# Kernel optimization log

Hardware: AMD Instinct MI355X
Metric: run time of the kernel (lower is better)

## Reference

```python
import jax, jax.numpy as jnp
import numpy as np

BSZ, DIM, SEQ_A, SEQ_B = 16, 768, 1024, 1024


def setup_inputs() -> dict:
    key = jax.random.key(0)
    kA, kB, kU = jax.random.split(key, 3)
    input_A = jax.random.normal(kA, (BSZ, DIM, SEQ_A), dtype=jnp.float32)
    input_B = jax.random.normal(kB, (BSZ, DIM, SEQ_B), dtype=jnp.float32)
    intput_msk = jnp.zeros((BSZ, SEQ_A, SEQ_B), dtype=jnp.float32)  # 0 = on, -inf = off
    U = jax.random.normal(kU, (DIM, DIM), dtype=jnp.float32)
    return {"input_A": input_A, "input_B": input_B, "intput_msk": intput_msk, "U": U}


def reference(input_A, input_B, intput_msk, U):
    # align[b,s,t] = tanh( A[b,:,s]^T U B[b,:,t] )  -> (bsz, seq_A, seq_B)
    align = jnp.einsum("bds,de,bet->bst", input_A, U, input_B)
    align = jnp.tanh(align) + intput_msk
    # per-token scores: max over the other modality's sequence, then softmax
    score_A = jax.nn.softmax(jnp.max(align, axis=2), axis=-1)  # (bsz, seq_A)
    score_B = jax.nn.softmax(jnp.max(align, axis=1), axis=-1)  # (bsz, seq_B)
    output_A = jnp.einsum("bds,bs->bd", input_A, score_A)  # (bsz, dim_A)
    output_B = jnp.einsum("bdt,bt->bd", input_B, score_B)  # (bsz, dim_B)
    return (output_A, output_B)
```

## Files before the change

### kernel.cpp

```cpp
#include <hip/hip_runtime.h>
#include <math.h>

#define BSZ  16
#define DIM  768
#define SEQA 1024
#define SEQB 1024

typedef float f32x4 __attribute__((ext_vector_type(4)));
typedef long long llong;

__device__ inline void gload_lds16(const void* g, void* l) {
    __builtin_amdgcn_global_load_lds(
        (const __attribute__((address_space(1))) void*)g,
        (__attribute__((address_space(3))) void*)l, 16, 0, 0);
}

__device__ inline unsigned enc_key(float f) {
    unsigned u = __float_as_uint(f);
    return (u & 0x80000000u) ? ~u : (u | 0x80000000u);
}
__device__ inline float dec_key(unsigned k) {
    return (k & 0x80000000u) ? __uint_as_float(k ^ 0x80000000u) : __uint_as_float(~k);
}

__device__ inline unsigned pk4_fp8(float a, float b, float c, float d) {
    int v = 0;
    v = __builtin_amdgcn_cvt_pk_fp8_f32(a, b, v, false);
    v = __builtin_amdgcn_cvt_pk_fp8_f32(c, d, v, true);
    return (unsigned)v;
}
__device__ inline unsigned char f2fp8(float a) {
    return (unsigned char)(__builtin_amdgcn_cvt_pk_fp8_f32(a, a, 0, false) & 0xFF);
}
__device__ inline unsigned short f2bf(float f) {
    unsigned u = __float_as_uint(f);
    return (unsigned short)((u + 0x7FFF + ((u >> 16) & 1)) >> 16);
}
__device__ inline float bf2f(unsigned short h) {
    return __uint_as_float((unsigned)h << 16);
}

__device__ inline float fast_tanh(float x) {
    float ax = fabsf(x);
    float u = __expf(-2.0f * ax);
    float th = __fdividef(1.0f - u, 1.0f + u);
    return copysignf(th, x);
}

__global__ __launch_bounds__(256) void t_cast_AB(const float* __restrict__ A,
                                                 const float* __restrict__ B,
                                                 unsigned char* __restrict__ At,
                                                 unsigned char* __restrict__ Bt,
                                                 unsigned short* __restrict__ At16,
                                                 unsigned short* __restrict__ Bt16,
                                                 int w16) {
    __shared__ float tl[64][68];
    const int z = blockIdx.z;
    const float* X = (z < BSZ) ? A : B;
    unsigned char* Y = (z < BSZ) ? At : Bt;
    unsigned short* Y16 = (z < BSZ) ? At16 : Bt16;
    const int b = z & 15;
    const int d0 = blockIdx.y * 64;
    const int s0 = blockIdx.x * 64;
    const int tid = threadIdx.x;
    const int rr = tid >> 4, c4 = tid & 15;
    const float* Xb = X + ((size_t)b * DIM + d0) * SEQA + s0;
#pragma unroll
    for (int i = 0; i < 4; i++) {
        int row = i * 16 + rr;
        float4 v = *(const float4*)&Xb[(size_t)row * SEQA + c4 * 4];
        *(float4*)&tl[row][c4 * 4] = v;
    }
    __syncthreads();
    const int m = tid & 15, sl = tid >> 4;
    unsigned char* Yb = Y + ((size_t)b * SEQA + s0) * DIM + d0;
#pragma unroll
    for (int i = 0; i < 4; i++) {
        int s = sl + 16 * i;
        unsigned v = pk4_fp8(tl[4 * m + 0][s], tl[4 * m + 1][s], tl[4 * m + 2][s], tl[4 * m + 3][s]);
        *(unsigned*)&Yb[(size_t)s * DIM + 4 * m] = v;
    }
    if (w16) {
        unsigned short* Yc = Y16 + ((size_t)b * SEQA + s0) * DIM + d0;
#pragma unroll
        for (int i = 0; i < 4; i++) {
            int s = sl + 16 * i;
            uint2 w;
            w.x = (unsigned)f2bf(tl[4 * m + 0][s]) | ((unsigned)f2bf(tl[4 * m + 1][s]) << 16);
            w.y = (unsigned)f2bf(tl[4 * m + 2][s]) | ((unsigned)f2bf(tl[4 * m + 3][s]) << 16);
            *(uint2*)&Yc[(size_t)s * DIM + 4 * m] = w;
        }
    }
}

__global__ __launch_bounds__(256) void t_cast_U(const float* __restrict__ U,
                                                unsigned char* __restrict__ Ut,
                                                unsigned* __restrict__ keyA,
                                                unsigned* __restrict__ keyB) {
    __shared__ float tl[64][68];
    const int d0 = blockIdx.y * 64;
    const int e0 = blockIdx.x * 64;
    const int tid = threadIdx.x;
    const int bid = blockIdx.y * gridDim.x + blockIdx.x;
    if (bid < 64) {
        int i = bid * 256 + tid;
        keyA[i] = 0u;
        keyB[i] = 0u;
    }
    const int rr = tid >> 4, c4 = tid & 15;
#pragma unroll
    for (int i = 0; i < 4; i++) {
        int row = i * 16 + rr;
        float4 v = *(const float4*)&U[(size_t)(d0 + row) * DIM + e0 + c4 * 4];
        *(float4*)&tl[row][c4 * 4] = v;
    }
    __syncthreads();
    const int m = tid & 15, sl = tid >> 4;
#pragma unroll
    for (int i = 0; i < 4; i++) {
        int e = sl + 16 * i;
        unsigned v = pk4_fp8(tl[4 * m + 0][e], tl[4 * m + 1][e], tl[4 * m + 2][e], tl[4 * m + 3][e]);
        *(unsigned*)&Ut[(size_t)(e0 + e) * DIM + d0 + 4 * m] = v;
    }
}

__device__ inline void stage64(const unsigned char* __restrict__ src, int kbyte0,
                               unsigned char* buf, int wid, int lane) {
    const int grow = lane >> 1;
    const int gcol = ((lane & 1) ^ ((lane >> 3) & 1)) * 16;
#pragma unroll
    for (int h = 0; h < 2; ++h)
        gload_lds16(src + (size_t)(wid * 32 + grow) * DIM + kbyte0 + 32 * h + gcol,
                    buf + h * 4096 + wid * 1024 + lane * 16);
}
__device__ inline llong frag64(const unsigned char* buf, int rowbase, int l15,
                               int quad, int h) {
    int koff = (((quad >> 1) ^ ((l15 >> 2) & 1)) << 4) + (quad & 1) * 8;
    return *(const llong*)(buf + h * 4096 + (rowbase + l15) * 32 + koff);
}

#define NK (DIM / 64)

__global__ __launch_bounds__(256) void k1_ua(const unsigned char* __restrict__ At,
                                             const unsigned char* __restrict__ Ut,
                                             unsigned char* __restrict__ Ct) {
    __shared__ __align__(16) unsigned char As[2][8192];
    __shared__ __align__(16) unsigned char Us[2][8192];
    const int b  = blockIdx.z;
    const int s0 = blockIdx.x * 128;
    const int e0 = blockIdx.y * 128;
    const int tid = threadIdx.x;
    const int lane = tid & 63;
    const int wid = tid >> 6;
    const int wr = wid >> 1, wc = wid & 1;
    const int quad = lane >> 4, l15 = lane & 15;

    const unsigned char* Ab = At + (size_t)(b * SEQA + s0) * DIM;
    const unsigned char* Ub = Ut + (size_t)e0 * DIM;
    f32x4 acc[4][4] = {};

#define K_COMPUTE(BUF)                                                               \
    {                                                                                \
        _Pragma("unroll") for (int h = 0; h < 2; ++h) {                              \
            llong av[4], bv[4];                                                      \
            _Pragma("unroll") for (int i = 0; i < 4; ++i)                            \
                av[i] = frag64(As[BUF], wr * 64 + 16 * i, l15, quad, h);             \
            _Pragma("unroll") for (int j = 0; j < 4; ++j)                            \
                bv[j] = frag64(Us[BUF], wc * 64 + 16 * j, l15, quad, h);             \
            _Pragma("unroll") for (int i = 0; i < 4; ++i)                            \
                _Pragma("unroll") for (int j = 0; j < 4; ++j)                        \
                    acc[i][j] = __builtin_amdgcn_mfma_f32_16x16x32_fp8_fp8(          \
                        av[i], bv[j], acc[i][j], 0, 0, 0);                           \
        }                                                                            \
    }

    stage64(Ab, 0, As[0], wid, lane);
    stage64(Ub, 0, Us[0], wid, lane);
    __syncthreads();
    for (int it = 0; it < NK; it += 2) {
        stage64(Ab, (it + 1) * 64, As[1], wid, lane);
        stage64(Ub, (it + 1) * 64, Us[1], wid, lane);
        K_COMPUTE(0);
        __syncthreads();
        if (it + 2 < NK) {
            stage64(Ab, (it + 2) * 64, As[0], wid, lane);
            stage64(Ub, (it + 2) * 64, Us[0], wid, lane);
        }
        K_COMPUTE(1);
        __syncthreads();
    }
    unsigned char* Cb = Ct + (size_t)b * SEQA * DIM;
#pragma unroll
    for (int i = 0; i < 4; ++i)
#pragma unroll
        for (int j = 0; j < 4; ++j) {
            int e_g = e0 + wc * 64 + 16 * j + l15;
#pragma unroll
            for (int r = 0; r < 4; ++r) {
                int s_g = s0 + wr * 64 + 16 * i + quad * 4 + r;
                Cb[(size_t)s_g * DIM + e_g] = f2fp8(acc[i][j][r]);
            }
        }
}

__global__ __launch_bounds__(256) void k2_align(const unsigned char* __restrict__ Ct,
                                                const unsigned char* __restrict__ Bt,
                                                const float* __restrict__ msk,
                                                unsigned* __restrict__ keyA,
                                                unsigned* __restrict__ keyB) {
    __shared__ __align__(16) unsigned char As[2][8192];
    __shared__ __align__(16) unsigned char Us[2][8192];
    const int b  = blockIdx.z;
    const int t0 = blockIdx.x * 128;
    const int s0 = blockIdx.y * 128;
    const int tid = threadIdx.x;
    const int lane = tid & 63;
    const int wid = tid >> 6;
    const int wr = wid >> 1, wc = wid & 1;
    const int quad = lane >> 4, l15 = lane & 15;

    const unsigned char* Bb = Bt + (size_t)(b * SEQB + t0) * DIM;
    const unsigned char* Cb = Ct + (size_t)(b * SEQA + s0) * DIM;
    f32x4 acc[4][4] = {};

    stage64(Bb, 0, As[0], wid, lane);
    stage64(Cb, 0, Us[0], wid, lane);
    __syncthreads();
    for (int it = 0; it < NK; it += 2) {
        stage64(Bb, (it + 1) * 64, As[1], wid, lane);
        stage64(Cb, (it + 1) * 64, Us[1], wid, lane);
        K_COMPUTE(0);
        __syncthreads();
        if (it + 2 < NK) {
            stage64(Bb, (it + 2) * 64, As[0], wid, lane);
            stage64(Cb, (it + 2) * 64, Us[0], wid, lane);
        }
        K_COMPUTE(1);
        __syncthreads();
    }

    const float* Mb = msk + (size_t)b * SEQA * SEQB;
#pragma unroll
    for (int i = 0; i < 4; ++i)
#pragma unroll
        for (int j = 0; j < 4; ++j) {
            int s_g = s0 + wc * 64 + 16 * j + l15;
            int t_g = t0 + wr * 64 + 16 * i + quad * 4;
            float4 mv = *(const float4*)&Mb[(size_t)s_g * SEQB + t_g];
            acc[i][j][0] = fast_tanh(acc[i][j][0]) + mv.x;
            acc[i][j][1] = fast_tanh(acc[i][j][1]) + mv.y;
            acc[i][j][2] = fast_tanh(acc[i][j][2]) + mv.z;
            acc[i][j][3] = fast_tanh(acc[i][j][3]) + mv.w;
        }
#pragma unroll
    for (int j = 0; j < 4; ++j) {
        float m = -INFINITY;
#pragma unroll
        for (int i = 0; i < 4; ++i)
#pragma unroll
            for (int r = 0; r < 4; ++r) m = fmaxf(m, acc[i][j][r]);
        m = fmaxf(m, __shfl_xor(m, 16));
        m = fmaxf(m, __shfl_xor(m, 32));
        if (quad == 0)
            atomicMax(&keyA[b * SEQA + s0 + wc * 64 + 16 * j + l15], enc_key(m));
    }
#pragma unroll
    for (int i = 0; i < 4; ++i)
#pragma unroll
        for (int r = 0; r < 4; ++r) {
            float m = fmaxf(fmaxf(acc[i][0][r], acc[i][1][r]), fmaxf(acc[i][2][r], acc[i][3][r]));
            m = fmaxf(m, __shfl_xor(m, 1));
            m = fmaxf(m, __shfl_xor(m, 2));
            m = fmaxf(m, __shfl_xor(m, 4));
            m = fmaxf(m, __shfl_xor(m, 8));
            if (l15 == 0)
                atomicMax(&keyB[b * SEQB + t0 + wr * 64 + 16 * i + quad * 4 + r], enc_key(m));
        }
}

__global__ __launch_bounds__(256) void k3_softmax(const unsigned* __restrict__ keyA,
                                                  const unsigned* __restrict__ keyB,
                                                  float* __restrict__ scoreA,
                                                  float* __restrict__ scoreB) {
    const int b = blockIdx.x;
    const bool isA = (blockIdx.y == 0);
    const unsigned* keys = isA ? (keyA + b * SEQA) : (keyB + b * SEQB);
    float* score = isA ? (scoreA + b * SEQA) : (scoreB + b * SEQB);
    __shared__ float sh[4];
    const int tid = threadIdx.x;
    float m[4];
    float mx = -INFINITY;
#pragma unroll
    for (int k = 0; k < 4; k++) {
        m[k] = dec_key(keys[tid + 256 * k]);
        mx = fmaxf(mx, m[k]);
    }
#pragma unroll
    for (int o = 32; o > 0; o >>= 1) mx = fmaxf(mx, __shfl_down(mx, o, 64));
    if ((tid & 63) == 0) sh[tid >> 6] = mx;
    __syncthreads();
    mx = fmaxf(fmaxf(sh[0], sh[1]), fmaxf(sh[2], sh[3]));
    __syncthreads();
    float e[4];
    float sum = 0.f;
#pragma unroll
    for (int k = 0; k < 4; k++) { e[k] = expf(m[k] - mx); sum += e[k]; }
#pragma unroll
    for (int o = 32; o > 0; o >>= 1) sum += __shfl_down(sum, o, 64);
    if ((tid & 63) == 0) sh[tid >> 6] = sum;
    __syncthreads();
    sum = sh[0] + sh[1] + sh[2] + sh[3];
    float inv = 1.0f / sum;
#pragma unroll
    for (int k = 0; k < 4; k++) score[tid + 256 * k] = e[k] * inv;
}

__global__ __launch_bounds__(256) void k4_bf16(const unsigned short* __restrict__ At16,
                                               const unsigned short* __restrict__ Bt16,
                                               const float* __restrict__ scoreA,
                                               const float* __restrict__ scoreB,
                                               float* __restrict__ out) {
    const int sc = blockIdx.x;
    const int which = blockIdx.y;
    const int b = blockIdx.z;
    const unsigned short* X = which ? Bt16 : At16;
    const float* S = which ? scoreB : scoreA;
    __shared__ float sh[128];
    const int tid = threadIdx.x;
    if (tid < 128) sh[tid] = S[b * SEQA + sc * 128 + tid];
    __syncthreads();
    const unsigned short* Xb = X + ((size_t)b * SEQA + sc * 128) * DIM;
    float a0 = 0.f, a1 = 0.f, a2 = 0.f;
    for (int s = 0; s < 128; ++s) {
        float f = sh[s];
        const unsigned short* row = Xb + (size_t)s * DIM;
        a0 += f * bf2f(row[tid]);
        a1 += f * bf2f(row[tid + 256]);
        a2 += f * bf2f(row[tid + 512]);
    }
    float* o = out + which * (BSZ * DIM) + b * DIM;
    atomicAdd(&o[tid], a0);
    atomicAdd(&o[tid + 256], a1);
    atomicAdd(&o[tid + 512], a2);
}

__global__ __launch_bounds__(256) void k4_f32(const float* __restrict__ A,
                                              const float* __restrict__ B,
                                              const float* __restrict__ scoreA,
                                              const float* __restrict__ scoreB,
                                              float* __restrict__ out) {
    const int which = blockIdx.y;
    const int row = blockIdx.x * 4 + (threadIdx.x >> 6);
    const int lane = threadIdx.x & 63;
    const float* X = which ? B : A;
    const float* S = which ? scoreB : scoreA;
    const int b = row / DIM;
    const float4* xr = (const float4*)(X + (size_t)row * SEQA);
    const float4* sr = (const float4*)(S + (size_t)b * SEQA);
    float acc = 0.f;
#pragma unroll
    for (int q = lane; q < SEQA / 4; q += 64) {
        float4 x = xr[q];
        float4 s = sr[q];
        acc += x.x * s.x + x.y * s.y + x.z * s.z + x.w * s.w;
    }
#pragma unroll
    for (int o = 32; o > 0; o >>= 1) acc += __shfl_down(acc, o, 64);
    if (lane == 0) out[which * (BSZ * DIM) + row] = acc;
}

extern "C" void kernel_launch(void* const* d_in, const int* in_sizes, int n_in,
                              void* d_out, int out_size, void* d_ws, size_t ws_size,
                              hipStream_t stream) {
    const float* A   = (const float*)d_in[0];
    const float* B   = (const float*)d_in[1];
    const float* msk = (const float*)d_in[2];
    const float* U   = (const float*)d_in[3];
    float* out = (float*)d_out;

    char* ws = (char*)d_ws;
    unsigned char* At = (unsigned char*)ws;
    unsigned char* Bt = (unsigned char*)(ws + 12582912);
    unsigned char* Ct = (unsigned char*)(ws + 25165824);
    unsigned char* Ut = (unsigned char*)(ws + 37748736);
    unsigned* keyA   = (unsigned*)(ws + 38338560);
    unsigned* keyB   = (unsigned*)(ws + 38404096);
    float*    scoreA = (float*)   (ws + 38469632);
    float*    scoreB = (float*)   (ws + 38535168);
    unsigned short* At16 = (unsigned short*)(ws + 38600704);
    unsigned short* Bt16 = (unsigned short*)(ws + 63766528);
    const int w16 = (ws_size >= 88932352ull) ? 1 : 0;

    t_cast_U<<<dim3(DIM / 64, DIM / 64, 1), 256, 0, stream>>>(U, Ut, keyA, keyB);
    t_cast_AB<<<dim3(SEQA / 64, DIM / 64, 2 * BSZ), 256, 0, stream>>>(A, B, At, Bt, At16, Bt16, w16);
    k1_ua<<<dim3(SEQA / 128, DIM / 128, BSZ), 256, 0, stream>>>(At, Ut, Ct);
    k2_align<<<dim3(SEQB / 128, SEQA / 128, BSZ), 256, 0, stream>>>(Ct, Bt, msk, keyA, keyB);
    k3_softmax<<<dim3(BSZ, 2), 256, 0, stream>>>(keyA, keyB, scoreA, scoreB);
    if (w16) {
        hipMemsetAsync(d_out, 0, (size_t)out_size * sizeof(float), stream);
        k4_bf16<<<dim3(8, 2, BSZ), 256, 0, stream>>>(At16, Bt16, scoreA, scoreB, out);
    } else {
        k4_f32<<<dim3(BSZ * DIM / 4, 2), 256, 0, stream>>>(A, B, scoreA, scoreB, out);
    }
}
```

Before: 256.7 us.

## Replace direct-to-LDS 64-byte staging with register-prefetched 256-byte K chunks

Both FP8 GEMM kernels move from double-buffered 64-byte K steps loaded with global_load_lds to 256-byte K chunks. Each chunk is prefetched into registers while MFMAs run on the current LDS tile, then written into an XOR-swizzled LDS layout. This cuts the number of barriers and loop iterations per tile, but raises register pressure and LDS use to 64 KB per block, which may lower occupancy. The k1 grid is also reordered so that e varies fastest across blocks, aiming for better L2 reuse of the A rows.

```diff
diff --git a/kernel.cpp b/kernel.cpp
--- a/kernel.cpp
+++ b/kernel.cpp
@@ -8,12 +8,6 @@
 
 typedef float f32x4 __attribute__((ext_vector_type(4)));
 typedef long long llong;
-
-__device__ inline void gload_lds16(const void* g, void* l) {
-    __builtin_amdgcn_global_load_lds(
-        (const __attribute__((address_space(1))) void*)g,
-        (__attribute__((address_space(3))) void*)l, 16, 0, 0);
-}
 
 __device__ inline unsigned enc_key(float f) {
     unsigned u = __float_as_uint(f);
@@ -124,31 +118,38 @@
     }
 }
 
-__device__ inline void stage64(const unsigned char* __restrict__ src, int kbyte0,
-                               unsigned char* buf, int wid, int lane) {
-    const int grow = lane >> 1;
-    const int gcol = ((lane & 1) ^ ((lane >> 3) & 1)) * 16;
-#pragma unroll
-    for (int h = 0; h < 2; ++h)
-        gload_lds16(src + (size_t)(wid * 32 + grow) * DIM + kbyte0 + 32 * h + gcol,
-                    buf + h * 4096 + wid * 1024 + lane * 16);
-}
-__device__ inline llong frag64(const unsigned char* buf, int rowbase, int l15,
-                               int quad, int h) {
-    int koff = (((quad >> 1) ^ ((l15 >> 2) & 1)) << 4) + (quad & 1) * 8;
-    return *(const llong*)(buf + h * 4096 + (rowbase + l15) * 32 + koff);
-}
-
-#define NK (DIM / 64)
+__device__ inline void ldchunk(const unsigned char* __restrict__ src, int kb0,
+                               uint4* g, int wid, int lane) {
+    const int r = wid * 32 + (lane >> 4);
+    const int gb = (lane & 15) * 16;
+#pragma unroll
+    for (int p = 0; p < 8; ++p)
+        g[p] = *(const uint4*)(src + (size_t)(r + p * 4) * DIM + kb0 + gb);
+}
+__device__ inline void stchunk(const uint4* g, unsigned char* lds, int wid, int lane) {
+    const int r = wid * 32 + (lane >> 4);
+    const int gg = lane & 15;
+#pragma unroll
+    for (int p = 0; p < 8; ++p) {
+        int row = r + p * 4;
+        *(uint4*)(lds + row * 256 + ((gg ^ (row & 15)) << 4)) = g[p];
+    }
+}
+__device__ inline llong frag256(const unsigned char* lds, int rowbase, int l15,
+                                int quad, int kk) {
+    int row = rowbase + l15;
+    int g = 2 * kk + (quad >> 1);
+    return *(const llong*)(lds + row * 256 + ((g ^ (row & 15)) << 4) + (quad & 1) * 8);
+}
 
 __global__ __launch_bounds__(256) void k1_ua(const unsigned char* __restrict__ At,
                                              const unsigned char* __restrict__ Ut,
                                              unsigned char* __restrict__ Ct) {
-    __shared__ __align__(16) unsigned char As[2][8192];
-    __shared__ __align__(16) unsigned char Us[2][8192];
+    __shared__ __align__(16) unsigned char As[128 * 256];
+    __shared__ __align__(16) unsigned char Us[128 * 256];
     const int b  = blockIdx.z;
-    const int s0 = blockIdx.x * 128;
-    const int e0 = blockIdx.y * 128;
+    const int e0 = blockIdx.x * 128;
+    const int s0 = blockIdx.y * 128;
     const int tid = threadIdx.x;
     const int lane = tid & 63;
     const int wid = tid >> 6;
@@ -157,37 +158,39 @@
 
     const unsigned char* Ab = At + (size_t)(b * SEQA + s0) * DIM;
     const unsigned char* Ub = Ut + (size_t)e0 * DIM;
+
+    uint4 ga[8], gu[8];
+    ldchunk(Ab, 0, ga, wid, lane);
+    ldchunk(Ub, 0, gu, wid, lane);
+    stchunk(ga, As, wid, lane);
+    stchunk(gu, Us, wid, lane);
+    __syncthreads();
+
     f32x4 acc[4][4] = {};
-
-#define K_COMPUTE(BUF)                                                               \
-    {                                                                                \
-        _Pragma("unroll") for (int h = 0; h < 2; ++h) {                              \
-            llong av[4], bv[4];                                                      \
-            _Pragma("unroll") for (int i = 0; i < 4; ++i)                            \
-                av[i] = frag64(As[BUF], wr * 64 + 16 * i, l15, quad, h);             \
-            _Pragma("unroll") for (int j = 0; j < 4; ++j)                            \
-                bv[j] = frag64(Us[BUF], wc * 64 + 16 * j, l15, quad, h);             \
-            _Pragma("unroll") for (int i = 0; i < 4; ++i)                            \
-                _Pragma("unroll") for (int j = 0; j < 4; ++j)                        \
-                    acc[i][j] = __builtin_amdgcn_mfma_f32_16x16x32_fp8_fp8(          \
-                        av[i], bv[j], acc[i][j], 0, 0, 0);                           \
-        }                                                                            \
-    }
-
-    stage64(Ab, 0, As[0], wid, lane);
-    stage64(Ub, 0, Us[0], wid, lane);
-    __syncthreads();
-    for (int it = 0; it < NK; it += 2) {
-        stage64(Ab, (it + 1) * 64, As[1], wid, lane);
-        stage64(Ub, (it + 1) * 64, Us[1], wid, lane);
-        K_COMPUTE(0);
-        __syncthreads();
-        if (it + 2 < NK) {
-            stage64(Ab, (it + 2) * 64, As[0], wid, lane);
-            stage64(Ub, (it + 2) * 64, Us[0], wid, lane);
-        }
-        K_COMPUTE(1);
-        __syncthreads();
+    for (int it = 0; it < 3; ++it) {
+        if (it < 2) {
+            ldchunk(Ab, (it + 1) * 256, ga, wid, lane);
+            ldchunk(Ub, (it + 1) * 256, gu, wid, lane);
+        }
+#pragma unroll
+        for (int kk = 0; kk < 8; ++kk) {
+            llong av[4], bv[4];
+#pragma unroll
+            for (int i = 0; i < 4; ++i) av[i] = frag256(As, wr * 64 + 16 * i, l15, quad, kk);
+#pragma unroll
+            for (int j = 0; j < 4; ++j) bv[j] = frag256(Us, wc * 64 + 16 * j, l15, quad, kk);
+#pragma unroll
+            for (int i = 0; i < 4; ++i)
+#pragma unroll
+                for (int j = 0; j < 4; ++j)
+                    acc[i][j] = __builtin_amdgcn_mfma_f32_16x16x32_fp8_fp8(av[i], bv[j], acc[i][j], 0, 0, 0);
+        }
+        if (it < 2) {
+            __syncthreads();
+            stchunk(ga, As, wid, lane);
+            stchunk(gu, Us, wid, lane);
+            __syncthreads();
+        }
     }
     unsigned char* Cb = Ct + (size_t)b * SEQA * DIM;
 #pragma unroll
@@ -208,8 +211,8 @@
                                                 const float* __restrict__ msk,
                                                 unsigned* __restrict__ keyA,
                                                 unsigned* __restrict__ keyB) {
-    __shared__ __align__(16) unsigned char As[2][8192];
-    __shared__ __align__(16) unsigned char Us[2][8192];
+    __shared__ __align__(16) unsigned char Bs[128 * 256];
+    __shared__ __align__(16) unsigned char Cs[128 * 256];
     const int b  = blockIdx.z;
     const int t0 = blockIdx.x * 128;
     const int s0 = blockIdx.y * 128;
@@ -221,22 +224,39 @@
 
     const unsigned char* Bb = Bt + (size_t)(b * SEQB + t0) * DIM;
     const unsigned char* Cb = Ct + (size_t)(b * SEQA + s0) * DIM;
+
+    uint4 gb[8], gc[8];
+    ldchunk(Bb, 0, gb, wid, lane);
+    ldchunk(Cb, 0, gc, wid, lane);
+    stchunk(gb, Bs, wid, lane);
+    stchunk(gc, Cs, wid, lane);
+    __syncthreads();
+
     f32x4 acc[4][4] = {};
-
-    stage64(Bb, 0, As[0], wid, lane);
-    stage64(Cb, 0, Us[0], wid, lane);
-    __syncthreads();
-    for (int it = 0; it < NK; it += 2) {
-        stage64(Bb, (it + 1) * 64, As[1], wid, lane);
-        stage64(Cb, (it + 1) * 64, Us[1], wid, lane);
-        K_COMPUTE(0);
-        __syncthreads();
-        if (it + 2 < NK) {
-            stage64(Bb, (it + 2) * 64, As[0], wid, lane);
-            stage64(Cb, (it + 2) * 64, Us[0], wid, lane);
-        }
-        K_COMPUTE(1);
-        __syncthreads();
+    for (int it = 0; it < 3; ++it) {
+        if (it < 2) {
+            ldchunk(Bb, (it + 1) * 256, gb, wid, lane);
+            ldchunk(Cb, (it + 1) * 256, gc, wid, lane);
+        }
+#pragma unroll
+        for (int kk = 0; kk < 8; ++kk) {
+            llong av[4], bv[4];
+#pragma unroll
+            for (int i = 0; i < 4; ++i) av[i] = frag256(Bs, wr * 64 + 16 * i, l15, quad, kk);
+#pragma unroll
+            for (int j = 0; j < 4; ++j) bv[j] = frag256(Cs, wc * 64 + 16 * j, l15, quad, kk);
+#pragma unroll
+            for (int i = 0; i < 4; ++i)
+#pragma unroll
+                for (int j = 0; j < 4; ++j)
+                    acc[i][j] = __builtin_amdgcn_mfma_f32_16x16x32_fp8_fp8(av[i], bv[j], acc[i][j], 0, 0, 0);
+        }
+        if (it < 2) {
+            __syncthreads();
+            stchunk(gb, Bs, wid, lane);
+            stchunk(gc, Cs, wid, lane);
+            __syncthreads();
+        }
     }
 
     const float* Mb = msk + (size_t)b * SEQA * SEQB;
@@ -393,7 +413,7 @@
 
     t_cast_U<<<dim3(DIM / 64, DIM / 64, 1), 256, 0, stream>>>(U, Ut, keyA, keyB);
     t_cast_AB<<<dim3(SEQA / 64, DIM / 64, 2 * BSZ), 256, 0, stream>>>(A, B, At, Bt, At16, Bt16, w16);
-    k1_ua<<<dim3(SEQA / 128, DIM / 128, BSZ), 256, 0, stream>>>(At, Ut, Ct);
+    k1_ua<<<dim3(DIM / 128, SEQA / 128, BSZ), 256, 0, stream>>>(At, Ut, Ct);
     k2_align<<<dim3(SEQB / 128, SEQA / 128, BSZ), 256, 0, stream>>>(Ct, Bt, msk, keyA, keyB);
     k3_softmax<<<dim3(BSZ, 2), 256, 0, stream>>>(keyA, keyB, scoreA, scoreB);
     if (w16) {
```

Result: slower. 352.8 us (+37.4%).
